# Performance work log

Measured on AMD Instinct MI355X. Metric: run time of the kernel, lower is better.

Reference implementation:

```python
import jax, jax.numpy as jnp
import numpy as np

N_NODES = 50000
N_EDGES = 1600000
IN_DIM = 128
OUT_DIM = 128
NUM_HEADS = 4
HEAD_DIM = OUT_DIM // NUM_HEADS


def setup_inputs() -> dict:
    key = jax.random.key(0)
    ks = jax.random.split(key, 10)
    s_in = 1.0 / np.sqrt(IN_DIM)
    s_out = 1.0 / np.sqrt(OUT_DIM)
    return {
        "x": jax.random.normal(ks[0], (N_NODES, IN_DIM), dtype=jnp.float32),
        "edge_index": jax.random.randint(ks[1], (2, N_EDGES), 0, N_NODES, dtype=jnp.int64),
        "Wq": jax.random.uniform(ks[2], (OUT_DIM, IN_DIM), jnp.float32, -s_in, s_in),
        "bq": jax.random.uniform(ks[3], (OUT_DIM,), jnp.float32, -s_in, s_in),
        "Wk": jax.random.uniform(ks[4], (OUT_DIM, IN_DIM), jnp.float32, -s_in, s_in),
        "bk": jax.random.uniform(ks[5], (OUT_DIM,), jnp.float32, -s_in, s_in),
        "Wv": jax.random.uniform(ks[6], (OUT_DIM, IN_DIM), jnp.float32, -s_in, s_in),
        "bv": jax.random.uniform(ks[7], (OUT_DIM,), jnp.float32, -s_in, s_in),
        "Wo": jax.random.uniform(ks[8], (OUT_DIM, OUT_DIM), jnp.float32, -s_out, s_out),
        "bo": jax.random.uniform(ks[9], (OUT_DIM,), jnp.float32, -s_out, s_out),
    }


def reference(x, edge_index, Wq, bq, Wk, bk, Wv, bv, Wo, bo):
    n = x.shape[0]
    # node-level projections -> [N, H, Hd]
    Q = (x @ Wq.T + bq).reshape(n, NUM_HEADS, HEAD_DIM)
    K = (x @ Wk.T + bk).reshape(n, NUM_HEADS, HEAD_DIM)
    V = (x @ Wv.T + bv).reshape(n, NUM_HEADS, HEAD_DIM)
    src, dst = edge_index[0], edge_index[1]
    # edge scores: [E, H]
    scores = (Q[dst] * K[src]).sum(-1) / np.sqrt(HEAD_DIM).astype(np.float32)
    # global-max shifted exp (faithful to original, which uses a single global max)
    scores_exp = jnp.exp(scores - scores.max())
    # per-dst normalization: [N, H]
    scores_sum = jax.ops.segment_sum(scores_exp, dst, num_segments=n)
    attention = scores_exp / (scores_sum[dst] + 1e-8)  # dropout in eval mode = identity
    # weighted aggregate of V[src] into dst: [N, H, Hd]
    messages = V[src] * attention[:, :, None]
    out = jax.ops.segment_sum(messages, dst, num_segments=n)
    out = out.reshape(n, OUT_DIM) @ Wo.T + bo
    return jax.nn.relu(out)
```

## Files before the change

### kernel.cpp

```cpp
#include <hip/hip_runtime.h>

#define N_NODES 50000
#define N_EDGES 1600000
#define DIM 128
#define M_PAD 50048
#define NBKT 196
#define CHUNK 6250
#define BB 256

#define OFF_WCATB  0UL
#define OFF_BCAT   98304UL
#define OFF_XB     99840UL
#define OFF_C      12912128UL
#define OFF_SRC    64112128UL
#define OFF_BKD    67312128UL
#define OFF_CNT    73712128UL
#define OFF_BSUM   73912832UL
#define OFF_BOFF   73913664UL
#define OFF_RS     73914496UL
#define OFF_AGG    74114560UL

typedef __attribute__((ext_vector_type(8))) short short8;
typedef __attribute__((ext_vector_type(4))) float floatx4;
typedef __attribute__((ext_vector_type(2))) float fx2;

__device__ __forceinline__ unsigned bf16r(float f) {
    unsigned u = __float_as_uint(f);
    return (u + 0x7fffu + ((u >> 16) & 1u)) >> 16;
}
__device__ __forceinline__ unsigned pack2(float a, float b) {
    return bf16r(a) | (bf16r(b) << 16);
}
__device__ __forceinline__ float blo(unsigned v) { return __uint_as_float(v << 16); }
__device__ __forceinline__ float bhi(unsigned v) { return __uint_as_float(v & 0xffff0000u); }

#define CVT_NB 6250
#define PREPW_NB 192
#define PREP_GRID (BB + CVT_NB + PREPW_NB)
__global__ __launch_bounds__(256) void k_prep(const float* __restrict__ x,
                                              unsigned short* __restrict__ xb,
                                              const float* __restrict__ Wq, const float* __restrict__ bq,
                                              const float* __restrict__ Wk, const float* __restrict__ bk,
                                              const float* __restrict__ Wv, const float* __restrict__ bv,
                                              unsigned short* __restrict__ Wcatb,
                                              float* __restrict__ bcat,
                                              const int* __restrict__ dstA,
                                              int* __restrict__ cnt) {
    __shared__ int h[NBKT];
    int bx = blockIdx.x, t = threadIdx.x;
    if (bx < BB) {
        if (t < NBKT) h[t] = 0;
        __syncthreads();
        int base = bx * CHUNK;
        for (int i = t; i < CHUNK; i += 256)
            atomicAdd(&h[dstA[base + i] >> 8], 1);
        __syncthreads();
        if (t < NBKT) cnt[t * BB + bx] = h[t];
    } else if (bx < BB + CVT_NB) {
        int i = (bx - BB) * 256 + t;
        if (i < N_NODES * DIM / 4) {
            float4 f = ((const float4*)x)[i];
            ushort4 o;
            o.x = (unsigned short)bf16r(f.x); o.y = (unsigned short)bf16r(f.y);
            o.z = (unsigned short)bf16r(f.z); o.w = (unsigned short)bf16r(f.w);
            ((ushort4*)xb)[i] = o;
        }
    } else {
        int i = (bx - BB - CVT_NB) * 256 + t;
        if (i < 3 * DIM * DIM) {
            int ro = i >> 7, col = i & 127;
            const float* W = (ro < 128) ? Wq : (ro < 256) ? Wk : Wv;
            Wcatb[i] = (unsigned short)bf16r(W[(ro & 127) * DIM + col]);
        }
        if (i < 3 * DIM) {
            const float* b = (i < 128) ? bq : (i < 256) ? bk : bv;
            bcat[i] = b[i & 127];
        }
    }
}

__global__ __launch_bounds__(256) void k_b2a(const int* __restrict__ cnt, int* __restrict__ bsum) {
    __shared__ int red[256];
    int t = threadIdx.x;
    red[t] = cnt[blockIdx.x * BB + t];
    __syncthreads();
    for (int off = 128; off > 0; off >>= 1) {
        if (t < off) red[t] += red[t + off];
        __syncthreads();
    }
    if (t == 0) bsum[blockIdx.x] = red[0];
}
__global__ __launch_bounds__(256) void k_b2b(const int* __restrict__ bsum, int* __restrict__ bktoff) {
    __shared__ int s[256];
    int t = threadIdx.x;
    int v = (t < NBKT) ? bsum[t] : 0;
    s[t] = v;
    __syncthreads();
    for (int off = 1; off < 256; off <<= 1) {
        int u = (t >= off) ? s[t - off] : 0;
        __syncthreads();
        s[t] += u;
        __syncthreads();
    }
    if (t < NBKT) bktoff[t] = s[t] - v;
    if (t == NBKT - 1) bktoff[NBKT] = s[t];
}
__global__ __launch_bounds__(256) void k_b2c(int* __restrict__ cnt, const int* __restrict__ bktoff) {
    __shared__ int s[256];
    int t = threadIdx.x;
    int v = cnt[blockIdx.x * BB + t];
    s[t] = v;
    __syncthreads();
    for (int off = 1; off < 256; off <<= 1) {
        int u = (t >= off) ? s[t - off] : 0;
        __syncthreads();
        s[t] += u;
        __syncthreads();
    }
    cnt[blockIdx.x * BB + t] = bktoff[blockIdx.x] + s[t] - v;
}

#define GQ_MB (M_PAD / 64)
#define GQ_BLOCKS (GQ_MB * 6)
#define GB3_GRPS 261
#define GB3_GRID (GB3_GRPS * 19)
__global__ __launch_bounds__(256) void k_gemmqkv_b3(const unsigned short* __restrict__ xb,
                                                    const unsigned short* __restrict__ Wb,
                                                    const float* __restrict__ bias,
                                                    unsigned* __restrict__ Cu, int M,
                                                    const int* __restrict__ srcA,
                                                    const int* __restrict__ dstA,
                                                    const int* __restrict__ cnt,
                                                    unsigned* __restrict__ bucketed) {
    __shared__ __align__(16) unsigned short As[64][136];
    __shared__ __align__(16) unsigned short Bs[64][136];
    __shared__ int cur[NBKT];
    const int grp = blockIdx.x / 19, r = blockIdx.x % 19;
    const int t = threadIdx.x;
    if (r == 18) {
        if (grp < BB) {
            if (t < NBKT) cur[t] = cnt[t * BB + grp];
            __syncthreads();
            int base = grp * CHUNK;
            for (int i = t; i < CHUNK; i += 256) {
                int e = base + i;
                int d = dstA[e];
                int p = atomicAdd(&cur[d >> 8], 1);
                bucketed[p] = (unsigned)srcA[e] | ((unsigned)(d & 255) << 16);
            }
        }
        return;
    }
    const int g = grp * 18 + r;
    if (g >= GQ_BLOCKS) return;
    const int m0 = (g % GQ_MB) * 64, n0 = (g / GQ_MB) * 64;
    {
        int row = t >> 2, ch = t & 3;
        const uint4* xrow = (const uint4*)(xb + (long)(m0 + row) * 128);
        const uint4* wrow = (const uint4*)(Wb + (long)(n0 + row) * 128);
#pragma unroll
        for (int j = 0; j < 4; ++j) {
            *(uint4*)&As[row][(ch + 4 * j) * 8] = xrow[ch + 4 * j];
            *(uint4*)&Bs[row][(ch + 4 * j) * 8] = wrow[ch + 4 * j];
        }
    }
    __syncthreads();
    const int w = t >> 6, lane = t & 63;
    const int quad = lane >> 4, c = lane & 15;
    floatx4 acc[4] = {{0.f,0.f,0.f,0.f},{0.f,0.f,0.f,0.f},{0.f,0.f,0.f,0.f},{0.f,0.f,0.f,0.f}};
#pragma unroll
    for (int ks = 0; ks < 4; ++ks) {
        short8 a = *(const short8*)&As[w * 16 + c][ks * 32 + quad * 8];
#pragma unroll
        for (int nt = 0; nt < 4; ++nt) {
            short8 b = *(const short8*)&Bs[nt * 16 + c][ks * 32 + quad * 8];
            acc[nt] = __builtin_amdgcn_mfma_f32_16x16x32_bf16(a, b, acc[nt], 0, 0, 0);
        }
    }
#pragma unroll
    for (int nt = 0; nt < 4; ++nt) {
        int gn = n0 + nt * 16 + c;
        float bv = bias[gn];
        int slice = gn >> 7;
        int cs = gn & 127;
#pragma unroll
        for (int i = 0; i < 4; ++i) {
            int gm = m0 + w * 16 + quad * 4 + i;
            float o = acc[nt][i] + bv;
            float f1 = __shfl_xor(o, 1);
            float f2 = __shfl_xor(o, 2);
            float f3 = __shfl_xor(o, 3);
            if (gm < M) {
                unsigned* crow = Cu + (long)gm * 256;
                if (slice == 0) {
                    ((float*)crow)[cs] = o;
                } else if (slice == 1) {
                    if ((c & 3) == 0) {
                        int pk = __builtin_amdgcn_cvt_pk_fp8_f32(o, f1, 0, false);
                        pk = __builtin_amdgcn_cvt_pk_fp8_f32(f2, f3, pk, true);
                        crow[128 + 3 * (cs >> 2)] = (unsigned)pk;
                    }
                } else {
                    if ((c & 1) == 0) {
                        int j = cs >> 1;
                        crow[128 + 3 * (j >> 1) + 1 + (j & 1)] = pack2(o, f1);
                    }
                }
            }
        }
    }
}

__global__ __launch_bounds__(256) void k_b4(const unsigned* __restrict__ bucketed,
                                            const int* __restrict__ bktoff,
                                            unsigned short* __restrict__ csr_src,
                                            int* __restrict__ row_start) {
    __shared__ int h[256], s[256], cur[256];
    int b = blockIdx.x, t = threadIdx.x;
    int base = bktoff[b], end = bktoff[b + 1];
    h[t] = 0;
    __syncthreads();
    for (int p = base + t; p < end; p += 256)
        atomicAdd(&h[bucketed[p] >> 16], 1);
    __syncthreads();
    int v = h[t];
    s[t] = v;
    __syncthreads();
    for (int off = 1; off < 256; off <<= 1) {
        int u = (t >= off) ? s[t - off] : 0;
        __syncthreads();
        s[t] += u;
        __syncthreads();
    }
    int start = base + s[t] - v;
    int d = b * 256 + t;
    if (d < N_NODES) row_start[d] = start;
    if (d == N_NODES - 1) row_start[N_NODES] = N_EDGES;
    cur[t] = start;
    __syncthreads();
    for (int p = base + t; p < end; p += 256) {
        unsigned u = bucketed[p];
        int q = atomicAdd(&cur[u >> 16], 1);
        csr_src[q] = (unsigned short)(u & 0xffffu);
    }
}

__global__ __launch_bounds__(256) void k_attn(const unsigned* __restrict__ Cu,
                                              const int* __restrict__ row_start,
                                              const unsigned short* __restrict__ csr_src,
                                              float* __restrict__ agg) {
    int d = blockIdx.x * 4 + (threadIdx.x >> 6);
    int lane = threadIdx.x & 63;
    if (d >= N_NODES) return;
    const int half = lane >> 5, sl = lane & 31;
    const float scale = 0.17677669529663687f;
    float4 q4 = *(const float4*)((const float*)(Cu + (long)d * 256) + 4 * sl);
    q4.x *= scale; q4.y *= scale; q4.z *= scale; q4.w *= scale;
    int s0 = row_start[d], s1 = row_start[d + 1];
    float lsum = 0.f, a0 = 0.f, a1 = 0.f, a2 = 0.f, a3 = 0.f;
    const int kvoff = 128 + 3 * sl;
    int pos = s0;
    for (; pos + 8 <= s1; pos += 8) {
        int base = pos + half * 4;
        int sa = csr_src[base + 0];
        int sb = csr_src[base + 1];
        int sc2 = csr_src[base + 2];
        int sd = csr_src[base + 3];
        const unsigned* ra = Cu + (long)sa * 256 + kvoff;
        const unsigned* rb = Cu + (long)sb * 256 + kvoff;
        const unsigned* rc = Cu + (long)sc2 * 256 + kvoff;
        const unsigned* rd = Cu + (long)sd * 256 + kvoff;
        unsigned ka = ra[0];
        unsigned kb = rb[0];
        unsigned kc = rc[0];
        unsigned kd = rd[0];
        uint2 va; va.x = ra[1]; va.y = ra[2];
        uint2 vb; vb.x = rb[1]; vb.y = rb[2];
        uint2 vc; vc.x = rc[1]; vc.y = rc[2];
        uint2 vd; vd.x = rd[1]; vd.y = rd[2];
        fx2 a01 = __builtin_amdgcn_cvt_pk_f32_fp8((int)ka, false);
        fx2 a23 = __builtin_amdgcn_cvt_pk_f32_fp8((int)ka, true);
        fx2 b01 = __builtin_amdgcn_cvt_pk_f32_fp8((int)kb, false);
        fx2 b23 = __builtin_amdgcn_cvt_pk_f32_fp8((int)kb, true);
        fx2 c01 = __builtin_amdgcn_cvt_pk_f32_fp8((int)kc, false);
        fx2 c23 = __builtin_amdgcn_cvt_pk_f32_fp8((int)kc, true);
        fx2 d01 = __builtin_amdgcn_cvt_pk_f32_fp8((int)kd, false);
        fx2 d23 = __builtin_amdgcn_cvt_pk_f32_fp8((int)kd, true);
        float pa = q4.x * a01.x + q4.y * a01.y + q4.z * a23.x + q4.w * a23.y;
        float pb = q4.x * b01.x + q4.y * b01.y + q4.z * b23.x + q4.w * b23.y;
        float pc = q4.x * c01.x + q4.y * c01.y + q4.z * c23.x + q4.w * c23.y;
        float pd = q4.x * d01.x + q4.y * d01.y + q4.z * d23.x + q4.w * d23.y;
        pa += __shfl_xor(pa, 1); pa += __shfl_xor(pa, 2); pa += __shfl_xor(pa, 4);
        pb += __shfl_xor(pb, 1); pb += __shfl_xor(pb, 2); pb += __shfl_xor(pb, 4);
        pc += __shfl_xor(pc, 1); pc += __shfl_xor(pc, 2); pc += __shfl_xor(pc, 4);
        pd += __shfl_xor(pd, 1); pd += __shfl_xor(pd, 2); pd += __shfl_xor(pd, 4);
        float wa = __expf(pa), wb = __expf(pb), wc = __expf(pc), wd = __expf(pd);
        lsum += (wa + wb) + (wc + wd);
        a0 += wa * blo(va.x) + wb * blo(vb.x) + wc * blo(vc.x) + wd * blo(vd.x);
        a1 += wa * bhi(va.x) + wb * bhi(vb.x) + wc * bhi(vc.x) + wd * bhi(vd.x);
        a2 += wa * blo(va.y) + wb * blo(vb.y) + wc * blo(vc.y) + wd * blo(vd.y);
        a3 += wa * bhi(va.y) + wb * bhi(vb.y) + wc * bhi(vc.y) + wd * bhi(vd.y);
    }
    for (; pos < s1; pos += 2) {
        int e = pos + half;
        bool ok = e < s1;
        int sa = csr_src[ok ? e : (s1 - 1)];
        const unsigned* ra = Cu + (long)sa * 256 + kvoff;
        unsigned ka = ra[0];
        uint2 va; va.x = ra[1]; va.y = ra[2];
        fx2 a01 = __builtin_amdgcn_cvt_pk_f32_fp8((int)ka, false);
        fx2 a23 = __builtin_amdgcn_cvt_pk_f32_fp8((int)ka, true);
        float pa = q4.x * a01.x + q4.y * a01.y + q4.z * a23.x + q4.w * a23.y;
        pa += __shfl_xor(pa, 1); pa += __shfl_xor(pa, 2); pa += __shfl_xor(pa, 4);
        float wa = ok ? __expf(pa) : 0.f;
        lsum += wa;
        a0 += wa * blo(va.x);
        a1 += wa * bhi(va.x);
        a2 += wa * blo(va.y);
        a3 += wa * bhi(va.y);
    }
    lsum += __shfl_xor(lsum, 32);
    a0 += __shfl_xor(a0, 32);
    a1 += __shfl_xor(a1, 32);
    a2 += __shfl_xor(a2, 32);
    a3 += __shfl_xor(a3, 32);
    if (lane < 32) {
        float inv = 1.f / (lsum + 1e-8f);
        float4 o;
        o.x = a0 * inv; o.y = a1 * inv; o.z = a2 * inv; o.w = a3 * inv;
        *(float4*)&agg[(long)d * 128 + 4 * sl] = o;
    }
}

__global__ __launch_bounds__(256) void k_gemm(const float* __restrict__ A,
                                              const float* __restrict__ B,
                                              const float* __restrict__ bias,
                                              float* __restrict__ Cp, int M) {
    __shared__ __align__(16) unsigned short As[64][136];
    __shared__ __align__(16) unsigned short Bs[64][136];
    const int m0 = blockIdx.x * 64, n0 = blockIdx.y * 64;
    const int t = threadIdx.x;
    {
        int row = t >> 2, ch = t & 3;
        const float* arow = A + (long)(m0 + row) * 128;
        const float* brow = B + (long)(n0 + row) * 128;
        bool aok = (m0 + row) < M;
#pragma unroll
        for (int j = 0; j < 4; ++j) {
            int c8 = (ch + 4 * j) * 8;
            uint4 av = {0u, 0u, 0u, 0u};
            if (aok) {
                float4 f0 = *(const float4*)(arow + c8);
                float4 f1 = *(const float4*)(arow + c8 + 4);
                av.x = pack2(f0.x, f0.y); av.y = pack2(f0.z, f0.w);
                av.z = pack2(f1.x, f1.y); av.w = pack2(f1.z, f1.w);
            }
            *(uint4*)&As[row][c8] = av;
            float4 g0 = *(const float4*)(brow + c8);
            float4 g1 = *(const float4*)(brow + c8 + 4);
            uint4 bv;
            bv.x = pack2(g0.x, g0.y); bv.y = pack2(g0.z, g0.w);
            bv.z = pack2(g1.x, g1.y); bv.w = pack2(g1.z, g1.w);
            *(uint4*)&Bs[row][c8] = bv;
        }
    }
    __syncthreads();
    const int w = t >> 6, lane = t & 63;
    const int quad = lane >> 4, c = lane & 15;
    floatx4 acc[4] = {{0.f,0.f,0.f,0.f},{0.f,0.f,0.f,0.f},{0.f,0.f,0.f,0.f},{0.f,0.f,0.f,0.f}};
#pragma unroll
    for (int ks = 0; ks < 4; ++ks) {
        short8 a = *(const short8*)&As[w * 16 + c][ks * 32 + quad * 8];
#pragma unroll
        for (int nt = 0; nt < 4; ++nt) {
            short8 b = *(const short8*)&Bs[nt * 16 + c][ks * 32 + quad * 8];
            acc[nt] = __builtin_amdgcn_mfma_f32_16x16x32_bf16(a, b, acc[nt], 0, 0, 0);
        }
    }
#pragma unroll
    for (int nt = 0; nt < 4; ++nt) {
        int gn = n0 + nt * 16 + c;
        float bv = bias[gn];
#pragma unroll
        for (int i = 0; i < 4; ++i) {
            int gm = m0 + w * 16 + quad * 4 + i;
            if (gm < M) Cp[(long)gm * 128 + gn] = fmaxf(acc[nt][i] + bv, 0.f);
        }
    }
}

extern "C" void kernel_launch(void* const* d_in, const int* in_sizes, int n_in,
                              void* d_out, int out_size, void* d_ws, size_t ws_size,
                              hipStream_t stream) {
    const float* x  = (const float*)d_in[0];
    const int* edge = (const int*)d_in[1];
    const float* Wq = (const float*)d_in[2];
    const float* bq = (const float*)d_in[3];
    const float* Wk = (const float*)d_in[4];
    const float* bk = (const float*)d_in[5];
    const float* Wv = (const float*)d_in[6];
    const float* bv = (const float*)d_in[7];
    const float* Wo = (const float*)d_in[8];
    const float* bo = (const float*)d_in[9];
    float* out = (float*)d_out;

    char* ws = (char*)d_ws;
    unsigned short* Wcatb = (unsigned short*)(ws + OFF_WCATB);
    float* bcat      = (float*)(ws + OFF_BCAT);
    unsigned short* xb = (unsigned short*)(ws + OFF_XB);
    unsigned* Cu     = (unsigned*)(ws + OFF_C);
    unsigned short* csr_src = (unsigned short*)(ws + OFF_SRC);
    unsigned* bucketed = (unsigned*)(ws + OFF_BKD);
    int*   cnt       = (int*)(ws + OFF_CNT);
    int*   bsum      = (int*)(ws + OFF_BSUM);
    int*   bktoff    = (int*)(ws + OFF_BOFF);
    int*   row_start = (int*)(ws + OFF_RS);
    float* agg       = (float*)(ws + OFF_AGG);

    const int* srcA = edge;
    const int* dstA = edge + N_EDGES;

    k_prep<<<PREP_GRID, 256, 0, stream>>>(
        x, xb, Wq, bq, Wk, bk, Wv, bv, Wcatb, bcat, dstA, cnt);

    k_b2a<<<NBKT, 256, 0, stream>>>(cnt, bsum);
    k_b2b<<<1, 256, 0, stream>>>(bsum, bktoff);
    k_b2c<<<NBKT, 256, 0, stream>>>(cnt, bktoff);

    k_gemmqkv_b3<<<GB3_GRID, 256, 0, stream>>>(
        xb, Wcatb, bcat, Cu, N_NODES, srcA, dstA, cnt, bucketed);

    k_b4<<<NBKT, 256, 0, stream>>>(bucketed, bktoff, csr_src, row_start);

    k_attn<<<(N_NODES + 3) / 4, 256, 0, stream>>>(Cu, row_start, csr_src, agg);

    k_gemm<<<dim3((N_NODES + 63) / 64, 2), 256, 0, stream>>>(agg, Wo, bo, out, N_NODES);
}
```

Baseline: 275.1 us.

## Build CSR by direct global-atomic counting sort instead of two-level bucket sort

Replaces the two-pass bucketed counting sort (per-block shared-memory bucket histograms, a bucket scan, then a per-bucket local sort kernel) with a direct per-node degree histogram built from global atomics. A three-kernel scan turns it into row_start, and the edges are scattered straight into csr_src through per-node global atomic cursors. This removes the intermediate bucketed array and the k_b4 pass, at the cost of 1.6M contended global atomics in two places and a scattered 2-byte write pattern. Edge order within each row becomes nondeterministic, which changes summation order in the attention step.

Result: slower. 367.6 us (+33.6%).

```diff
diff --git a/kernel.cpp b/kernel.cpp
--- a/kernel.cpp
+++ b/kernel.cpp
@@ -4,17 +4,17 @@
 #define N_EDGES 1600000
 #define DIM 128
 #define M_PAD 50048
-#define NBKT 196
 #define CHUNK 6250
 #define BB 256
+#define SCAN_NB 196
 
 #define OFF_WCATB  0UL
 #define OFF_BCAT   98304UL
 #define OFF_XB     99840UL
 #define OFF_C      12912128UL
 #define OFF_SRC    64112128UL
-#define OFF_BKD    67312128UL
-#define OFF_CNT    73712128UL
+#define OFF_CUR    67312128UL
+#define OFF_DEG    73712128UL
 #define OFF_BSUM   73912832UL
 #define OFF_BOFF   73913664UL
 #define OFF_RS     73914496UL
@@ -45,17 +45,12 @@
                                               unsigned short* __restrict__ Wcatb,
                                               float* __restrict__ bcat,
                                               const int* __restrict__ dstA,
-                                              int* __restrict__ cnt) {
-    __shared__ int h[NBKT];
+                                              int* __restrict__ deg) {
     int bx = blockIdx.x, t = threadIdx.x;
     if (bx < BB) {
-        if (t < NBKT) h[t] = 0;
-        __syncthreads();
         int base = bx * CHUNK;
         for (int i = t; i < CHUNK; i += 256)
-            atomicAdd(&h[dstA[base + i] >> 8], 1);
-        __syncthreads();
-        if (t < NBKT) cnt[t * BB + bx] = h[t];
+            atomicAdd(&deg[dstA[base + i]], 1);
     } else if (bx < BB + CVT_NB) {
         int i = (bx - BB) * 256 + t;
         if (i < N_NODES * DIM / 4) {
@@ -79,21 +74,12 @@
     }
 }
 
-__global__ __launch_bounds__(256) void k_b2a(const int* __restrict__ cnt, int* __restrict__ bsum) {
-    __shared__ int red[256];
-    int t = threadIdx.x;
-    red[t] = cnt[blockIdx.x * BB + t];
-    __syncthreads();
-    for (int off = 128; off > 0; off >>= 1) {
-        if (t < off) red[t] += red[t + off];
-        __syncthreads();
-    }
-    if (t == 0) bsum[blockIdx.x] = red[0];
-}
-__global__ __launch_bounds__(256) void k_b2b(const int* __restrict__ bsum, int* __restrict__ bktoff) {
+__global__ __launch_bounds__(256) void k_scan1(const int* __restrict__ deg,
+                                               int* __restrict__ incl,
+                                               int* __restrict__ bsum) {
     __shared__ int s[256];
-    int t = threadIdx.x;
-    int v = (t < NBKT) ? bsum[t] : 0;
+    int t = threadIdx.x, i = blockIdx.x * 256 + t;
+    int v = (i < N_NODES) ? deg[i] : 0;
     s[t] = v;
     __syncthreads();
     for (int off = 1; off < 256; off <<= 1) {
@@ -102,13 +88,13 @@
         s[t] += u;
         __syncthreads();
     }
-    if (t < NBKT) bktoff[t] = s[t] - v;
-    if (t == NBKT - 1) bktoff[NBKT] = s[t];
-}
-__global__ __launch_bounds__(256) void k_b2c(int* __restrict__ cnt, const int* __restrict__ bktoff) {
+    if (i < N_NODES) incl[i] = s[t];
+    if (t == 255) bsum[blockIdx.x] = s[255];
+}
+__global__ __launch_bounds__(256) void k_scan2(const int* __restrict__ bsum, int* __restrict__ boff) {
     __shared__ int s[256];
     int t = threadIdx.x;
-    int v = cnt[blockIdx.x * BB + t];
+    int v = (t < SCAN_NB) ? bsum[t] : 0;
     s[t] = v;
     __syncthreads();
     for (int off = 1; off < 256; off <<= 1) {
@@ -117,7 +103,20 @@
         s[t] += u;
         __syncthreads();
     }
-    cnt[blockIdx.x * BB + t] = bktoff[blockIdx.x] + s[t] - v;
+    if (t < SCAN_NB) boff[t] = s[t] - v;
+    if (t == SCAN_NB - 1) boff[SCAN_NB] = s[t];
+}
+__global__ __launch_bounds__(256) void k_scan3(const int* __restrict__ deg,
+                                               const int* __restrict__ boff,
+                                               int* __restrict__ row_start,
+                                               int* __restrict__ cursor) {
+    int t = threadIdx.x, i = blockIdx.x * 256 + t;
+    if (i < N_NODES) {
+        int start = boff[blockIdx.x] + row_start[i] - deg[i];
+        row_start[i] = start;
+        cursor[i] = start;
+    }
+    if (i == N_NODES - 1) row_start[N_NODES] = N_EDGES;
 }
 
 #define GQ_MB (M_PAD / 64)
@@ -130,23 +129,20 @@
                                                     unsigned* __restrict__ Cu, int M,
                                                     const int* __restrict__ srcA,
                                                     const int* __restrict__ dstA,
-                                                    const int* __restrict__ cnt,
-                                                    unsigned* __restrict__ bucketed) {
+                                                    int* __restrict__ cursor,
+                                                    unsigned short* __restrict__ csr_src) {
     __shared__ __align__(16) unsigned short As[64][136];
     __shared__ __align__(16) unsigned short Bs[64][136];
-    __shared__ int cur[NBKT];
     const int grp = blockIdx.x / 19, r = blockIdx.x % 19;
     const int t = threadIdx.x;
     if (r == 18) {
         if (grp < BB) {
-            if (t < NBKT) cur[t] = cnt[t * BB + grp];
-            __syncthreads();
             int base = grp * CHUNK;
             for (int i = t; i < CHUNK; i += 256) {
                 int e = base + i;
                 int d = dstA[e];
-                int p = atomicAdd(&cur[d >> 8], 1);
-                bucketed[p] = (unsigned)srcA[e] | ((unsigned)(d & 255) << 16);
+                int q = atomicAdd(&cursor[d], 1);
+                csr_src[q] = (unsigned short)srcA[e];
             }
         }
         return;
@@ -208,40 +204,6 @@
                 }
             }
         }
-    }
-}
-
-__global__ __launch_bounds__(256) void k_b4(const unsigned* __restrict__ bucketed,
-                                            const int* __restrict__ bktoff,
-                                            unsigned short* __restrict__ csr_src,
-                                            int* __restrict__ row_start) {
-    __shared__ int h[256], s[256], cur[256];
-    int b = blockIdx.x, t = threadIdx.x;
-    int base = bktoff[b], end = bktoff[b + 1];
-    h[t] = 0;
-    __syncthreads();
-    for (int p = base + t; p < end; p += 256)
-        atomicAdd(&h[bucketed[p] >> 16], 1);
-    __syncthreads();
-    int v = h[t];
-    s[t] = v;
-    __syncthreads();
-    for (int off = 1; off < 256; off <<= 1) {
-        int u = (t >= off) ? s[t - off] : 0;
-        __syncthreads();
-        s[t] += u;
-        __syncthreads();
-    }
-    int start = base + s[t] - v;
-    int d = b * 256 + t;
-    if (d < N_NODES) row_start[d] = start;
-    if (d == N_NODES - 1) row_start[N_NODES] = N_EDGES;
-    cur[t] = start;
-    __syncthreads();
-    for (int p = base + t; p < end; p += 256) {
-        unsigned u = bucketed[p];
-        int q = atomicAdd(&cur[u >> 16], 1);
-        csr_src[q] = (unsigned short)(u & 0xffffu);
     }
 }
 
@@ -410,27 +372,27 @@
     unsigned short* xb = (unsigned short*)(ws + OFF_XB);
     unsigned* Cu     = (unsigned*)(ws + OFF_C);
     unsigned short* csr_src = (unsigned short*)(ws + OFF_SRC);
-    unsigned* bucketed = (unsigned*)(ws + OFF_BKD);
-    int*   cnt       = (int*)(ws + OFF_CNT);
+    int*   cursor    = (int*)(ws + OFF_CUR);
+    int*   deg       = (int*)(ws + OFF_DEG);
     int*   bsum      = (int*)(ws + OFF_BSUM);
-    int*   bktoff    = (int*)(ws + OFF_BOFF);
+    int*   boff      = (int*)(ws + OFF_BOFF);
     int*   row_start = (int*)(ws + OFF_RS);
     float* agg       = (float*)(ws + OFF_AGG);
 
     const int* srcA = edge;
     const int* dstA = edge + N_EDGES;
 
+    hipMemsetAsync(deg, 0, N_NODES * sizeof(int), stream);
+
     k_prep<<<PREP_GRID, 256, 0, stream>>>(
-        x, xb, Wq, bq, Wk, bk, Wv, bv, Wcatb, bcat, dstA, cnt);
-
-    k_b2a<<<NBKT, 256, 0, stream>>>(cnt, bsum);
-    k_b2b<<<1, 256, 0, stream>>>(bsum, bktoff);
-    k_b2c<<<NBKT, 256, 0, stream>>>(cnt, bktoff);
+        x, xb, Wq, bq, Wk, bk, Wv, bv, Wcatb, bcat, dstA, deg);
+
+    k_scan1<<<SCAN_NB, 256, 0, stream>>>(deg, row_start, bsum);
+    k_scan2<<<1, 256, 0, stream>>>(bsum, boff);
+    k_scan3<<<SCAN_NB, 256, 0, stream>>>(deg, boff, row_start, cursor);
 
     k_gemmqkv_b3<<<GB3_GRID, 256, 0, stream>>>(
-        xb, Wcatb, bcat, Cu, N_NODES, srcA, dstA, cnt, bucketed);
-
-    k_b4<<<NBKT, 256, 0, stream>>>(bucketed, bktoff, csr_src, row_start);
+        xb, Wcatb, bcat, Cu, N_NODES, srcA, dstA, cursor, csr_src);
 
     k_attn<<<(N_NODES + 3) / 4, 256, 0, stream>>>(Cu, row_start, csr_src, agg);
 
```
